# Performance work log

Measured on AMD Instinct MI355X. Metric: run time of the kernel, lower is better.

## Reference

```python
import jax, jax.numpy as jnp
import numpy as np

N_NODES = 20000
N_EDGES = 200000
N_GRAPHS = 128
IN_DIM = 16
EDGE_DIM = 8
HID = 64
OUT_DIM = 10


def setup_inputs() -> dict:
    key = jax.random.key(0)
    ks = jax.random.split(key, 16)
    s = lambda k, *shape: jax.random.normal(k, shape, dtype=jnp.float32) * 0.05
    edge_attr = jax.random.normal(ks[0], (N_EDGES, EDGE_DIM), dtype=jnp.float32)
    edge_index = jax.random.randint(ks[1], (2, N_EDGES), 0, N_NODES, dtype=jnp.int32)
    batch = jnp.sort(jax.random.randint(ks[2], (N_NODES,), 0, N_GRAPHS, dtype=jnp.int32))
    return {
        "edge_attr": edge_attr,
        "edge_index": edge_index,
        "batch": batch,
        # node embedding (single row, repeated since data.x is None)
        "node_emb": s(ks[3], 1, IN_DIM),
        # edge MLP: edge_dim -> hid -> hid -> in*hid
        "w1": s(ks[4], EDGE_DIM, HID), "b1": jnp.zeros((HID,), jnp.float32),
        "w2": s(ks[5], HID, HID), "b2": jnp.zeros((HID,), jnp.float32),
        "w3": s(ks[6], HID, IN_DIM * HID), "b3": jnp.zeros((IN_DIM * HID,), jnp.float32),
        # NNConv root weight (Linear, bias=False) and conv bias
        "root_w": s(ks[7], IN_DIM, HID),
        "conv_b": jnp.zeros((HID,), jnp.float32),
        # classifier head: hid -> 2*hid -> out
        "l1_w": s(ks[8], HID, 2 * HID), "l1_b": jnp.zeros((2 * HID,), jnp.float32),
        "l2_w": s(ks[9], 2 * HID, OUT_DIM), "l2_b": jnp.zeros((OUT_DIM,), jnp.float32),
    }


def reference(edge_attr, edge_index, batch, node_emb, w1, b1, w2, b2, w3, b3,
              root_w, conv_b, l1_w, l1_b, l2_w, l2_b):
    # node features: single embedding row repeated for every node
    x = jnp.broadcast_to(node_emb, (N_NODES, IN_DIM))  # [N, in]

    # edge MLP -> dynamic per-edge weight matrices [E, in, hid]
    h = jax.nn.relu(edge_attr @ w1 + b1)
    h = jax.nn.relu(h @ w2 + b2)
    theta = (h @ w3 + b3).reshape(N_EDGES, IN_DIM, HID)

    src, dst = edge_index[0], edge_index[1]
    # per-edge matmul: gather source features, apply edge weight
    msg = jnp.einsum('ei,eih->eh', x[src], theta)  # [E, hid]
    # scatter-add aggregate at destination nodes
    agg = jax.ops.segment_sum(msg, dst, num_segments=N_NODES)  # [N, hid]

    # NNConv root transform + bias, then relu
    out = jax.nn.relu(agg + x @ root_w + conv_b)  # [N, hid]

    # global mean pool per graph
    sums = jax.ops.segment_sum(out, batch, num_segments=N_GRAPHS)  # [G, hid]
    counts = jax.ops.segment_sum(jnp.ones((N_NODES,), out.dtype), batch,
                                 num_segments=N_GRAPHS)
    pooled = sums / jnp.maximum(counts, 1.0)[:, None]

    # classifier head
    logits = jax.nn.relu(pooled @ l1_w + l1_b) @ l2_w + l2_b  # [G, out]
    return logits
```

## Files before the change

### kernel.cpp

```cpp
#include <hip/hip_runtime.h>
#include <hip/hip_bf16.h>
#include <hip/amd_detail/amd_hip_unsafe_atomics.h>

#define N_EDGES 200000
#define N_NODES 20000
#define N_GRAPHS 128
#define IN_DIM 16
#define EDGE_DIM 8
#define HID 64
#define OUT_DIM 10
#define SCAN_NBLK ((N_NODES + 1023) / 1024)
#define N_TILES (N_EDGES / 16)
#define TPW 2
#define N_EWAVES (N_TILES / TPW)

typedef __attribute__((ext_vector_type(8))) short bf16x8;
typedef __attribute__((ext_vector_type(4))) float f32x4;

__device__ __forceinline__ ushort f2bf(float x) {
    unsigned b = __float_as_uint(x);
    return (ushort)((b + 0x7FFFu + ((b >> 16) & 1u)) >> 16);
}
__device__ __forceinline__ float bf2f(ushort u) {
    return __uint_as_float(((unsigned)u) << 16);
}

__global__ __launch_bounds__(256) void combo_kernel(
    const float* __restrict__ emb, const float* __restrict__ w3,
    const float* __restrict__ b3, const float* __restrict__ root_w,
    const float* __restrict__ conv_b, const int* __restrict__ dst_idx,
    const float* __restrict__ w1, const float* __restrict__ w2,
    float* __restrict__ W3p, float* __restrict__ b3p, float* __restrict__ r,
    ushort* __restrict__ fw1, ushort* __restrict__ fw2,
    int* __restrict__ counts)
{
    if (blockIdx.x < 16) {
        int t = blockIdx.x * 256 + threadIdx.x;
        int k = t >> 6;
        int h = t & 63;
        float acc = 0.f;
#pragma unroll
        for (int i = 0; i < IN_DIM; ++i)
            acc = fmaf(emb[i], w3[k * (IN_DIM * HID) + i * HID + h], acc);
        W3p[t] = acc;
        if (t < HID) {
            float a = 0.f, rr = 0.f;
#pragma unroll
            for (int i = 0; i < IN_DIM; ++i) {
                a  = fmaf(emb[i], b3[i * HID + t], a);
                rr = fmaf(emb[i], root_w[i * HID + t], rr);
            }
            b3p[t] = a;
            r[t]   = rr + conv_b[t];
        }
    } else if (blockIdx.x < 64) {
        int idx  = (blockIdx.x - 16) * 256 + threadIdx.x;
        int frag = idx >> 9;
        int rem  = idx & 511;
        int lane = rem >> 3, i = rem & 7;
        int q = lane >> 4, n16 = lane & 15;
        if (frag < 8) {
            int t = frag >> 1, h = frag & 1;
            int k = 8 * q + i, n = t * 16 + n16;
            float v = (k < EDGE_DIM) ? w1[k * HID + n] : 0.f;
            ushort hi = f2bf(v);
            fw1[((t * 2 + h) * 64 + lane) * 8 + i] =
                (h == 0) ? hi : f2bf(v - bf2f(hi));
        } else {
            int u = frag - 8;
            int t = u >> 2, f = (u >> 1) & 1, h = u & 1;
            int k = f * 32 + 8 * q + i, n = t * 16 + n16;
            float v = w2[k * HID + n];
            ushort hi = f2bf(v);
            fw2[(((t * 2 + f) * 2 + h) * 64 + lane) * 8 + i] =
                (h == 0) ? hi : f2bf(v - bf2f(hi));
        }
    } else {
        int e = (blockIdx.x - 64) * 256 + threadIdx.x;
        if (e < N_EDGES) atomicAdd(&counts[dst_idx[e]], 1);
    }
}

__global__ __launch_bounds__(1024) void scanA_kernel(
    const int* __restrict__ counts, int* __restrict__ start, int* __restrict__ tot,
    const float* __restrict__ W3p, ushort* __restrict__ fw3)
{
    const int b = blockIdx.x, t = threadIdx.x;
    if (b >= SCAN_NBLK) {
        int idx  = (b - SCAN_NBLK) * 1024 + t;
        int u    = idx >> 9;
        int rem  = idx & 511;
        int lane = rem >> 3, i = rem & 7;
        int tt = u >> 2, f = (u >> 1) & 1, h = u & 1;
        int k = f * 32 + 8 * (lane >> 4) + i, n = tt * 16 + (lane & 15);
        float v = W3p[k * HID + n];
        ushort hi = f2bf(v);
        fw3[(((tt * 2 + f) * 2 + h) * 64 + lane) * 8 + i] =
            (h == 0) ? hi : f2bf(v - bf2f(hi));
        return;
    }
    const int i = b * 1024 + t;
    const int v = (i < N_NODES) ? counts[i] : 0;
    const int lane = t & 63, wid = t >> 6;
    __shared__ int wsum[16];
    int incl = v;
#pragma unroll
    for (int off = 1; off < 64; off <<= 1) {
        int u = __shfl_up(incl, off, 64);
        if (lane >= off) incl += u;
    }
    if (lane == 63) wsum[wid] = incl;
    __syncthreads();
    if (wid == 0) {
        int wv = (lane < 16) ? wsum[lane] : 0;
        int wi = wv;
#pragma unroll
        for (int off = 1; off < 16; off <<= 1) {
            int u = __shfl_up(wi, off, 64);
            if (lane >= off) wi += u;
        }
        if (lane < 16) wsum[lane] = wi - wv;
    }
    __syncthreads();
    const int excl = wsum[wid] + incl - v;
    if (i < N_NODES) start[i] = excl;
    if (t == 1023) tot[b] = excl + v;
}

__global__ __launch_bounds__(64) void scanB_kernel(int* __restrict__ tot,
                                                   int* __restrict__ off)
{
    const int t = threadIdx.x;
    int v = (t < SCAN_NBLK) ? tot[t] : 0;
    int incl = v;
#pragma unroll
    for (int o = 1; o < 64; o <<= 1) {
        int u = __shfl_up(incl, o, 64);
        if (t >= o) incl += u;
    }
    if (t < SCAN_NBLK) off[t] = incl - v;
}

__global__ __launch_bounds__(1024) void scanC_kernel(
    int* __restrict__ start, int* __restrict__ cursor, const int* __restrict__ off)
{
    const int b = blockIdx.x, t = threadIdx.x;
    const int i = b * 1024 + t;
    if (i < N_NODES) {
        const int s = start[i] + off[b];
        start[i]  = s;
        cursor[i] = s;
    }
    if (b == 0 && t == 0) start[N_NODES] = N_EDGES;
}

__global__ __launch_bounds__(256) void edge_mfma_kernel(
    const float* __restrict__ edge_attr, const int* __restrict__ dst_idx,
    const ushort* __restrict__ fw1, const ushort* __restrict__ fw2,
    const ushort* __restrict__ fw3,
    const float* __restrict__ b1, const float* __restrict__ b2,
    const float* __restrict__ b3p,
    int* __restrict__ cursor, float* __restrict__ msg_buf)
{
    const int lane = threadIdx.x & 63;
    const int wv   = threadIdx.x >> 6;
    const int gw   = blockIdx.x * 4 + wv;
    const int tile0 = gw * TPW;
    if (tile0 >= N_TILES) return;
    const int q = lane >> 4, l16 = lane & 15;

    __shared__ ushort s_hi[4][TPW][16][72];
    __shared__ ushort s_lo[4][TPW][16][72];

    float bb1[4], bb2[4], bb3[4];
#pragma unroll
    for (int t = 0; t < 4; ++t) {
        bb1[t] = b1[t * 16 + l16];
        bb2[t] = b2[t * 16 + l16];
        bb3[t] = b3p[t * 16 + l16];
    }

    float e8[TPW][8];
    int   p_mine[TPW];
#pragma unroll
    for (int tt = 0; tt < TPW; ++tt) {
        p_mine[tt] = 0;
#pragma unroll
        for (int i = 0; i < 8; ++i) e8[tt][i] = 0.f;
        if (lane < 16) {
            const long em = (long)(tile0 + tt) * 16 + lane;
            const float4 A = *(const float4*)&edge_attr[em * EDGE_DIM + 0];
            const float4 B = *(const float4*)&edge_attr[em * EDGE_DIM + 4];
            e8[tt][0] = A.x; e8[tt][1] = A.y; e8[tt][2] = A.z; e8[tt][3] = A.w;
            e8[tt][4] = B.x; e8[tt][5] = B.y; e8[tt][6] = B.z; e8[tt][7] = B.w;
            p_mine[tt] = atomicAdd(&cursor[dst_idx[em]], 1);
        }
    }

    {
        bf16x8 w1h[4], w1l[4];
#pragma unroll
        for (int t = 0; t < 4; ++t) {
            w1h[t] = ((const bf16x8*)fw1)[(t * 2 + 0) * 64 + lane];
            w1l[t] = ((const bf16x8*)fw1)[(t * 2 + 1) * 64 + lane];
        }
#pragma unroll
        for (int tt = 0; tt < TPW; ++tt) {
            bf16x8 a1h, a1l;
#pragma unroll
            for (int i = 0; i < 8; ++i) {
                const ushort hi = f2bf(e8[tt][i]);
                a1h[i] = (short)hi;
                a1l[i] = (short)f2bf(e8[tt][i] - bf2f(hi));
            }
#pragma unroll
            for (int t = 0; t < 4; ++t) {
                f32x4 c = {0.f, 0.f, 0.f, 0.f};
                c = __builtin_amdgcn_mfma_f32_16x16x32_bf16(a1l, w1h[t], c, 0, 0, 0);
                c = __builtin_amdgcn_mfma_f32_16x16x32_bf16(a1h, w1l[t], c, 0, 0, 0);
                c = __builtin_amdgcn_mfma_f32_16x16x32_bf16(a1h, w1h[t], c, 0, 0, 0);
#pragma unroll
                for (int rr = 0; rr < 4; ++rr) {
                    float x = fmaxf(c[rr] + bb1[t], 0.f);
                    const ushort hi = f2bf(x);
                    s_hi[wv][tt][q * 4 + rr][t * 16 + l16] = hi;
                    s_lo[wv][tt][q * 4 + rr][t * 16 + l16] = f2bf(x - bf2f(hi));
                }
            }
        }
    }

    {
        bf16x8 w2h[4][2], w2l[4][2];
#pragma unroll
        for (int t = 0; t < 4; ++t)
#pragma unroll
            for (int f = 0; f < 2; ++f) {
                w2h[t][f] = ((const bf16x8*)fw2)[((t * 2 + f) * 2 + 0) * 64 + lane];
                w2l[t][f] = ((const bf16x8*)fw2)[((t * 2 + f) * 2 + 1) * 64 + lane];
            }
#pragma unroll
        for (int tt = 0; tt < TPW; ++tt) {
            bf16x8 a2h[2], a2l[2];
#pragma unroll
            for (int f = 0; f < 2; ++f) {
                a2h[f] = *(const bf16x8*)&s_hi[wv][tt][l16][f * 32 + 8 * q];
                a2l[f] = *(const bf16x8*)&s_lo[wv][tt][l16][f * 32 + 8 * q];
            }
            f32x4 cc[4];
#pragma unroll
            for (int t = 0; t < 4; ++t) {
                f32x4 c = {0.f, 0.f, 0.f, 0.f};
#pragma unroll
                for (int f = 0; f < 2; ++f) {
                    c = __builtin_amdgcn_mfma_f32_16x16x32_bf16(a2l[f], w2h[t][f], c, 0, 0, 0);
                    c = __builtin_amdgcn_mfma_f32_16x16x32_bf16(a2h[f], w2l[t][f], c, 0, 0, 0);
                    c = __builtin_amdgcn_mfma_f32_16x16x32_bf16(a2h[f], w2h[t][f], c, 0, 0, 0);
                }
                cc[t] = c;
            }
#pragma unroll
            for (int t = 0; t < 4; ++t)
#pragma unroll
                for (int rr = 0; rr < 4; ++rr) {
                    float x = fmaxf(cc[t][rr] + bb2[t], 0.f);
                    const ushort hi = f2bf(x);
                    s_hi[wv][tt][q * 4 + rr][t * 16 + l16] = hi;
                    s_lo[wv][tt][q * 4 + rr][t * 16 + l16] = f2bf(x - bf2f(hi));
                }
        }
    }

    {
        bf16x8 w3h[4][2], w3l[4][2];
#pragma unroll
        for (int t = 0; t < 4; ++t)
#pragma unroll
            for (int f = 0; f < 2; ++f) {
                w3h[t][f] = ((const bf16x8*)fw3)[((t * 2 + f) * 2 + 0) * 64 + lane];
                w3l[t][f] = ((const bf16x8*)fw3)[((t * 2 + f) * 2 + 1) * 64 + lane];
            }
#pragma unroll
        for (int tt = 0; tt < TPW; ++tt) {
            bf16x8 a3h[2], a3l[2];
#pragma unroll
            for (int f = 0; f < 2; ++f) {
                a3h[f] = *(const bf16x8*)&s_hi[wv][tt][l16][f * 32 + 8 * q];
                a3l[f] = *(const bf16x8*)&s_lo[wv][tt][l16][f * 32 + 8 * q];
            }
            f32x4 cc[4];
#pragma unroll
            for (int t = 0; t < 4; ++t) {
                f32x4 c = {0.f, 0.f, 0.f, 0.f};
#pragma unroll
                for (int f = 0; f < 2; ++f) {
                    c = __builtin_amdgcn_mfma_f32_16x16x32_bf16(a3l[f], w3h[t][f], c, 0, 0, 0);
                    c = __builtin_amdgcn_mfma_f32_16x16x32_bf16(a3h[f], w3l[t][f], c, 0, 0, 0);
                    c = __builtin_amdgcn_mfma_f32_16x16x32_bf16(a3h[f], w3h[t][f], c, 0, 0, 0);
                }
                cc[t] = c;
            }
            int p_r[4];
#pragma unroll
            for (int rr = 0; rr < 4; ++rr)
                p_r[rr] = __shfl(p_mine[tt], q * 4 + rr);
#pragma unroll
            for (int t = 0; t < 4; ++t)
#pragma unroll
                for (int rr = 0; rr < 4; ++rr)
                    msg_buf[(long)p_r[rr] * HID + t * 16 + l16] = cc[t][rr] + bb3[t];
        }
    }
}

#define GN_PER_WAVE 8
__global__ __launch_bounds__(256) void gather_kernel(
    const float* __restrict__ msg_buf, const int* __restrict__ start,
    const float* __restrict__ r, const int* __restrict__ batch,
    float* __restrict__ sums, float* __restrict__ counts_f)
{
    const int wave = threadIdx.x >> 6;
    const int j    = threadIdx.x & 63;
    const int n0   = blockIdx.x * (4 * GN_PER_WAVE) + wave * GN_PER_WAVE;
    if (n0 >= N_NODES) return;
    const int n1 = min(n0 + GN_PER_WAVE, N_NODES);
    const float rj = r[j];

    int   g    = batch[n0];
    float pacc = 0.f, cnt = 0.f;
    for (int n = n0; n < n1; ++n) {
        const int gn = batch[n];
        if (gn != g) {
            unsafeAtomicAdd(&sums[g * HID + j], pacc);
            if (j == 0) unsafeAtomicAdd(&counts_f[g], cnt);
            g = gn; pacc = 0.f; cnt = 0.f;
        }
        float acc = 0.f;
        const int p0 = start[n], p1 = start[n + 1];
        for (int p = p0; p < p1; ++p)
            acc += msg_buf[(long)p * HID + j];
        pacc += fmaxf(acc + rj, 0.f);
        cnt  += 1.f;
    }
    unsafeAtomicAdd(&sums[g * HID + j], pacc);
    if (j == 0) unsafeAtomicAdd(&counts_f[g], cnt);
}

__global__ __launch_bounds__(128) void head_kernel(
    const float* __restrict__ sums, const float* __restrict__ counts,
    const float* __restrict__ l1_w, const float* __restrict__ l1_b,
    const float* __restrict__ l2_w, const float* __restrict__ l2_b,
    float* __restrict__ out)
{
    const int g = blockIdx.x;
    const int t = threadIdx.x;
    __shared__ float pooled[HID];
    __shared__ float hid[2 * HID];

    const float cnt = fmaxf(counts[g], 1.0f);
    if (t < HID) pooled[t] = sums[g * HID + t] / cnt;
    __syncthreads();

    float a = l1_b[t];
#pragma unroll
    for (int k = 0; k < HID; ++k)
        a = fmaf(pooled[k], l1_w[k * (2 * HID) + t], a);
    hid[t] = fmaxf(a, 0.f);
    __syncthreads();

    if (t < OUT_DIM) {
        float o = l2_b[t];
#pragma unroll
        for (int k = 0; k < 2 * HID; ++k)
            o = fmaf(hid[k], l2_w[k * OUT_DIM + t], o);
        out[g * OUT_DIM + t] = o;
    }
}

extern "C" void kernel_launch(void* const* d_in, const int* in_sizes, int n_in,
                              void* d_out, int out_size, void* d_ws, size_t ws_size,
                              hipStream_t stream) {
    const float* edge_attr = (const float*)d_in[0];
    const int*   edge_idx  = (const int*)d_in[1];
    const int*   batch     = (const int*)d_in[2];
    const float* node_emb  = (const float*)d_in[3];
    const float* w1        = (const float*)d_in[4];
    const float* b1        = (const float*)d_in[5];
    const float* w2        = (const float*)d_in[6];
    const float* b2        = (const float*)d_in[7];
    const float* w3        = (const float*)d_in[8];
    const float* b3        = (const float*)d_in[9];
    const float* root_w    = (const float*)d_in[10];
    const float* conv_b    = (const float*)d_in[11];
    const float* l1_w      = (const float*)d_in[12];
    const float* l1_b      = (const float*)d_in[13];
    const float* l2_w      = (const float*)d_in[14];
    const float* l2_b      = (const float*)d_in[15];
    float* out = (float*)d_out;

    float* ws     = (float*)d_ws;
    float* W3p    = ws;
    float* b3p    = W3p + HID * HID;
    float* r      = b3p + HID;
    float* sums   = r + HID;
    float* cts    = sums + N_GRAPHS * HID;
    int*   counts = (int*)(cts + N_GRAPHS);
    int*   startp = counts + N_NODES;
    int*   cursor = startp + (N_NODES + 1);
    int*   tot    = cursor + N_NODES;
    int*   off    = tot + SCAN_NBLK;
    ushort* fw1 = (ushort*)(((uintptr_t)(off + SCAN_NBLK) + 15) & ~(uintptr_t)15);
    ushort* fw2 = fw1 + 4096;
    ushort* fw3 = fw2 + 8192;
    float* msg  = (float*)(fw3 + 8192);

    hipMemsetAsync(sums, 0,
                   (size_t)(N_GRAPHS * HID + N_GRAPHS + N_NODES) * 4, stream);

    const int* dst_idx = edge_idx + N_EDGES;

    combo_kernel<<<64 + (N_EDGES + 255) / 256, 256, 0, stream>>>(
        node_emb, w3, b3, root_w, conv_b, dst_idx, w1, w2,
        W3p, b3p, r, fw1, fw2, counts);

    scanA_kernel<<<SCAN_NBLK + 8, 1024, 0, stream>>>(counts, startp, tot, W3p, fw3);
    scanB_kernel<<<1, 64, 0, stream>>>(tot, off);
    scanC_kernel<<<SCAN_NBLK, 1024, 0, stream>>>(startp, cursor, off);

    edge_mfma_kernel<<<(N_EWAVES + 3) / 4, 256, 0, stream>>>(
        edge_attr, dst_idx, fw1, fw2, fw3, b1, b2, b3p, cursor, msg);

    gather_kernel<<<(N_NODES + 4 * GN_PER_WAVE - 1) / (4 * GN_PER_WAVE), 256, 0, stream>>>(
        msg, startp, r, batch, sums, cts);

    head_kernel<<<N_GRAPHS, 128, 0, stream>>>(
        sums, cts, l1_w, l1_b, l2_w, l2_b, out);
}
```

Before: 97.34 us.

## Store edge messages as bf16 and fold block-offset scan into scanC

```diff
diff --git a/kernel.cpp b/kernel.cpp
--- a/kernel.cpp
+++ b/kernel.cpp
@@ -127,27 +127,21 @@
     if (t == 1023) tot[b] = excl + v;
 }
 
-__global__ __launch_bounds__(64) void scanB_kernel(int* __restrict__ tot,
-                                                   int* __restrict__ off)
-{
-    const int t = threadIdx.x;
-    int v = (t < SCAN_NBLK) ? tot[t] : 0;
-    int incl = v;
-#pragma unroll
-    for (int o = 1; o < 64; o <<= 1) {
-        int u = __shfl_up(incl, o, 64);
-        if (t >= o) incl += u;
-    }
-    if (t < SCAN_NBLK) off[t] = incl - v;
-}
-
 __global__ __launch_bounds__(1024) void scanC_kernel(
-    int* __restrict__ start, int* __restrict__ cursor, const int* __restrict__ off)
-{
+    int* __restrict__ start, int* __restrict__ cursor, const int* __restrict__ tot)
+{
+    __shared__ int s_off;
     const int b = blockIdx.x, t = threadIdx.x;
+    if (t < 64) {
+        int v = (t < b && t < SCAN_NBLK) ? tot[t] : 0;
+#pragma unroll
+        for (int o = 32; o >= 1; o >>= 1) v += __shfl_xor(v, o, 64);
+        if (t == 0) s_off = v;
+    }
+    __syncthreads();
     const int i = b * 1024 + t;
     if (i < N_NODES) {
-        const int s = start[i] + off[b];
+        const int s = start[i] + s_off;
         start[i]  = s;
         cursor[i] = s;
     }
@@ -160,7 +154,7 @@
     const ushort* __restrict__ fw3,
     const float* __restrict__ b1, const float* __restrict__ b2,
     const float* __restrict__ b3p,
-    int* __restrict__ cursor, float* __restrict__ msg_buf)
+    int* __restrict__ cursor, ushort* __restrict__ msg16)
 {
     const int lane = threadIdx.x & 63;
     const int wv   = threadIdx.x >> 6;
@@ -308,14 +302,15 @@
             for (int t = 0; t < 4; ++t)
 #pragma unroll
                 for (int rr = 0; rr < 4; ++rr)
-                    msg_buf[(long)p_r[rr] * HID + t * 16 + l16] = cc[t][rr] + bb3[t];
+                    msg16[(long)p_r[rr] * HID + t * 16 + l16] =
+                        f2bf(cc[t][rr] + bb3[t]);
         }
     }
 }
 
 #define GN_PER_WAVE 8
 __global__ __launch_bounds__(256) void gather_kernel(
-    const float* __restrict__ msg_buf, const int* __restrict__ start,
+    const ushort* __restrict__ msg16, const int* __restrict__ start,
     const float* __restrict__ r, const int* __restrict__ batch,
     float* __restrict__ sums, float* __restrict__ counts_f)
 {
@@ -338,7 +333,7 @@
         float acc = 0.f;
         const int p0 = start[n], p1 = start[n + 1];
         for (int p = p0; p < p1; ++p)
-            acc += msg_buf[(long)p * HID + j];
+            acc += bf2f(msg16[(long)p * HID + j]);
         pacc += fmaxf(acc + rj, 0.f);
         cnt  += 1.f;
     }
@@ -408,11 +403,10 @@
     int*   startp = counts + N_NODES;
     int*   cursor = startp + (N_NODES + 1);
     int*   tot    = cursor + N_NODES;
-    int*   off    = tot + SCAN_NBLK;
-    ushort* fw1 = (ushort*)(((uintptr_t)(off + SCAN_NBLK) + 15) & ~(uintptr_t)15);
+    ushort* fw1 = (ushort*)(((uintptr_t)(tot + SCAN_NBLK) + 15) & ~(uintptr_t)15);
     ushort* fw2 = fw1 + 4096;
     ushort* fw3 = fw2 + 8192;
-    float* msg  = (float*)(fw3 + 8192);
+    ushort* msg16 = fw3 + 8192;
 
     hipMemsetAsync(sums, 0,
                    (size_t)(N_GRAPHS * HID + N_GRAPHS + N_NODES) * 4, stream);
@@ -424,14 +418,13 @@
         W3p, b3p, r, fw1, fw2, counts);
 
     scanA_kernel<<<SCAN_NBLK + 8, 1024, 0, stream>>>(counts, startp, tot, W3p, fw3);
-    scanB_kernel<<<1, 64, 0, stream>>>(tot, off);
-    scanC_kernel<<<SCAN_NBLK, 1024, 0, stream>>>(startp, cursor, off);
+    scanC_kernel<<<SCAN_NBLK, 1024, 0, stream>>>(startp, cursor, tot);
 
     edge_mfma_kernel<<<(N_EWAVES + 3) / 4, 256, 0, stream>>>(
-        edge_attr, dst_idx, fw1, fw2, fw3, b1, b2, b3p, cursor, msg);
+        edge_attr, dst_idx, fw1, fw2, fw3, b1, b2, b3p, cursor, msg16);
 
     gather_kernel<<<(N_NODES + 4 * GN_PER_WAVE - 1) / (4 * GN_PER_WAVE), 256, 0, stream>>>(
-        msg, startp, r, batch, sums, cts);
+        msg16, startp, r, batch, sums, cts);
 
     head_kernel<<<N_GRAPHS, 128, 0, stream>>>(
         sums, cts, l1_w, l1_b, l2_w, l2_b, out);
```

Measured after the change: 94.42 us. 1.03x faster.
